# Kernel tuning notes

Hardware: AMD Instinct MI355X
Metric: run time of the kernel (lower is better)

The kernel has to match this reference:

```python
import jax, jax.numpy as jnp
import numpy as np

R0 = 1.0
N_NODES = 10000
N_EDGES = 160000
DIM_A, DIM_V, DIM_D, CHAN = 64, 32, 16, 16

# Levi-Civita tensor for the antisymmetric (cross-product-like) products
_EPS = np.zeros((3, 3, 3), dtype=np.float32)
for (i, j, k), s in (((0,1,2),1.),((1,2,0),1.),((2,0,1),1.),((0,2,1),-1.),((2,1,0),-1.),((1,0,2),-1.)):
    _EPS[i, j, k] = s


def _tl(W, x):
    """TensLinear: mix channel axis 1 of x (B, din, *(3,)*rank) with W (dout, din)."""
    y = jnp.tensordot(x, W, axes=((1,), (1,)))  # (B, *(3,)*rank, dout)
    return jnp.moveaxis(y, -1, 1)


def radial_encode_8(r, r0):
    # 8 Gaussian radial basis functions on |r|/r0
    d = jnp.linalg.norm(r, axis=-1)            # (E,)
    x = d * (8.0 / r0)
    mu = jnp.arange(8, dtype=r.dtype)
    return jnp.exp(-0.5 * (x[:, None] - mu[None, :]) ** 2)  # (E, 8)


def tens_sigmoid_1(v):
    # equivariant squashing: scale vector by tanh(|v|)/|v|
    n = jnp.linalg.norm(v, axis=-1, keepdims=True)
    return v * jnp.tanh(n) / (n + 1e-12)


def _forward(floats, src, dst, n_nodes):
    (r_ij, x_a, x_v, x_d, W_L0, W_L1, W_L2,
     W_Y000, W_Y110, W_Y220, W_Y011, W_Y101, W_Y121, W_Y211,
     W_Y022, W_Y202, W_Y112, W_Y222, W_Y111, W_Y212,
     W_enc, b_enc, W_dir, W1, b1, W2, b2, W3, b3) = floats
    eps = jnp.asarray(_EPS)
    rad = radial_encode_8(r_ij, R0) @ W_enc.T + b_enc        # (E, chan)
    r = tens_sigmoid_1(r_ij * (7.0 / R0))                    # (E, 3)
    phi_a = rad                                              # (E, chan)
    phi_v = rad[:, :, None] * r[:, None, :]                  # (E, chan, 3)
    phi_d = rad[:, :, None, None] * r[:, None, None, :] * r[:, None, :, None]  # (E, chan, 3, 3)
    # gather destination-node features per edge
    x_a_j = _tl(W_L0, x_a)[dst]                              # (E, chan)
    x_v_j = _tl(W_L1, x_v)[dst]                              # (E, chan, 3)
    x_d_j = _tl(W_L2, x_d)[dst]                              # (E, chan, 3, 3)
    # equivariant tensor products (Bee.apply)
    y_000 = x_a_j * phi_a
    y_110 = jnp.sum(x_v_j * phi_v, -1)
    y_220 = jnp.sum(x_d_j * phi_d, (-2, -1))
    y_011 = x_a_j[..., None] * phi_v
    y_101 = x_v_j * phi_a[..., None]
    y_121 = jnp.einsum('ecj,ecji->eci', x_v_j, phi_d)
    y_211 = jnp.einsum('ecij,ecj->eci', x_d_j, phi_v)
    y_022 = x_a_j[..., None, None] * phi_d
    y_202 = x_d_j * phi_a[..., None, None]
    y_112 = x_v_j[..., :, None] * phi_v[..., None, :]
    y_222 = jnp.einsum('ecik,eckj->ecij', x_d_j, phi_d)
    y_111 = jnp.cross(x_v_j, phi_v)
    y_212 = jnp.einsum('ikl,eckj,ecl->ecij', eps, x_d_j, phi_v)
    psi_a = _tl(W_Y000, y_000) + _tl(W_Y110, y_110) + _tl(W_Y220, y_220)
    psi_v = (_tl(W_Y011, y_011) + _tl(W_Y101, y_101) + _tl(W_Y121, y_121)
             + _tl(W_Y211, y_211) + _tl(W_Y111, y_111))
    psi_d = (_tl(W_Y022, y_022) + _tl(W_Y202, y_202) + _tl(W_Y112, y_112)
             + _tl(W_Y222, y_222) + _tl(W_Y212, y_212))
    # residual MLP on the scalar channel: lin_direct(x) + layers(x)
    lrelu = lambda x: jnp.where(x >= 0, x, 0.1 * x)
    h = lrelu(psi_a @ W1.T + b1)
    h = lrelu(h @ W2.T + b2)
    psi_a = psi_a + psi_a @ W_dir.T + (h @ W3.T + b3)
    # scatter-reduce messages to source nodes
    B_a = jax.ops.segment_sum(psi_a, src, num_segments=n_nodes)
    B_v = jax.ops.segment_sum(psi_v, src, num_segments=n_nodes)
    B_d = jax.ops.segment_sum(psi_d, src, num_segments=n_nodes)
    return 0.1 * B_a, 0.1 * B_v, 0.1 * B_d


def setup_inputs() -> dict:
    key = jax.random.key(0)
    ks = jax.random.split(key, 32)
    f32 = jnp.float32
    nrm = lambda k, shape, scale=1.0: scale * jax.random.normal(k, shape, dtype=f32)
    E, N = N_EDGES, N_NODES
    sC = CHAN ** -0.5
    inp = {
        'r_ij': nrm(ks[0], (E, 3)),
        'x_a': nrm(ks[1], (N, DIM_A)),
        'x_v': nrm(ks[2], (N, DIM_V, 3)),
        'x_d': nrm(ks[3], (N, DIM_D, 3, 3)),
        'W_L0': nrm(ks[4], (CHAN, DIM_A), DIM_A ** -0.5),
        'W_L1': nrm(ks[5], (CHAN, DIM_V), DIM_V ** -0.5),
        'W_L2': nrm(ks[6], (CHAN, DIM_D), DIM_D ** -0.5),
        'W_Y000': nrm(ks[7], (DIM_A, CHAN), sC),
        'W_Y110': nrm(ks[8], (DIM_A, CHAN), sC),
        'W_Y220': nrm(ks[9], (DIM_A, CHAN), sC),
        'W_Y011': nrm(ks[10], (DIM_V, CHAN), sC),
        'W_Y101': nrm(ks[11], (DIM_V, CHAN), sC),
        'W_Y121': nrm(ks[12], (DIM_V, CHAN), sC),
        'W_Y211': nrm(ks[13], (DIM_V, CHAN), sC),
        'W_Y022': nrm(ks[14], (DIM_D, CHAN), sC),
        'W_Y202': nrm(ks[15], (DIM_D, CHAN), sC),
        'W_Y112': nrm(ks[16], (DIM_D, CHAN), sC),
        'W_Y222': nrm(ks[17], (DIM_D, CHAN), sC),
        'W_Y111': nrm(ks[18], (DIM_V, CHAN), sC),
        'W_Y212': nrm(ks[19], (DIM_D, CHAN), sC),
        'W_enc': nrm(ks[20], (CHAN, 8), 8 ** -0.5),
        'b_enc': jnp.zeros((CHAN,), f32),
        'W_dir': nrm(ks[21], (DIM_A, DIM_A), DIM_A ** -0.5),
        'W1': nrm(ks[22], (2 * DIM_A, DIM_A), DIM_A ** -0.5),
        'b1': jnp.zeros((2 * DIM_A,), f32),
        'W2': nrm(ks[23], (2 * DIM_A, 2 * DIM_A), (2 * DIM_A) ** -0.5),
        'b2': jnp.zeros((2 * DIM_A,), f32),
        'W3': nrm(ks[24], (DIM_A, 2 * DIM_A), (2 * DIM_A) ** -0.5),
        'b3': jnp.zeros((DIM_A,), f32),
        'src': jax.random.randint(ks[25], (E,), 0, N, dtype=jnp.int32),
        'dst': jax.random.randint(ks[26], (E,), 0, N, dtype=jnp.int32),
        'n_nodes': N,
    }
    return inp


def reference(r_ij, x_a, x_v, x_d, W_L0, W_L1, W_L2, W_Y000, W_Y110, W_Y220,
              W_Y011, W_Y101, W_Y121, W_Y211, W_Y022, W_Y202, W_Y112, W_Y222,
              W_Y111, W_Y212, W_enc, b_enc, W_dir, W1, b1, W2, b2, W3, b3,
              src, dst, n_nodes):
    floats = (r_ij, x_a, x_v, x_d, W_L0, W_L1, W_L2, W_Y000, W_Y110, W_Y220,
              W_Y011, W_Y101, W_Y121, W_Y211, W_Y022, W_Y202, W_Y112, W_Y222,
              W_Y111, W_Y212, W_enc, b_enc, W_dir, W1, b1, W2, b2, W3, b3)
    return _forward(floats, src, dst, n_nodes)
```

## Files before the change

kernel.cpp:

```cpp
#include <hip/hip_runtime.h>
#include <hip/hip_bf16.h>

typedef __hip_bfloat16 bf16;
typedef __attribute__((ext_vector_type(8))) short bf16x8;
typedef __attribute__((ext_vector_type(4))) float f32x4;

__device__ __forceinline__ void st_bf16(short* p, float v) {
    uint32_t u = __float_as_uint(v) + 0x8000u;
    *p = (short)(u >> 16);
}
__device__ __forceinline__ float bb2f(short s) {
    uint32_t u = ((uint32_t)(uint16_t)s) << 16;
    return __uint_as_float(u);
}

__global__ __launch_bounds__(256) void prep_all(
    const float* __restrict__ W000, const float* __restrict__ W110, const float* __restrict__ W220,
    const float* __restrict__ W011, const float* __restrict__ W101, const float* __restrict__ W121,
    const float* __restrict__ W211, const float* __restrict__ W111,
    const float* __restrict__ W022, const float* __restrict__ W202, const float* __restrict__ W112,
    const float* __restrict__ W222, const float* __restrict__ W212,
    const float* __restrict__ W1, const float* __restrict__ W2, const float* __restrict__ W3,
    const float* __restrict__ Wdir, bf16* __restrict__ wout,
    const float* __restrict__ xa, const float* __restrict__ xv, const float* __restrict__ xd,
    const float* __restrict__ WL0, const float* __restrict__ WL1, const float* __restrict__ WL2,
    float* __restrict__ Pa, float* __restrict__ Pv, float* __restrict__ Pd, int N, int NPB,
    const int* __restrict__ src, const int* __restrict__ dst,
    int* __restrict__ cnt_s, int* __restrict__ cnt_d, int E)
{
    int b = blockIdx.x;
    const int tid = threadIdx.x;
    if (b < 178) {
        int i = b * 256 + tid;
        if (i >= 45568) return;
        float v = 0.f;
        if (i < 4096) {
            int o = i >> 6, k = i & 63;
            if (k < 48) {
                int t = k >> 4, c = k & 15;
                const float* W = (t == 0) ? W000 : (t == 1) ? W110 : W220;
                v = W[o * 16 + c];
            }
        } else if (i < 7168) {
            int r = i - 4096, ch = r / 96, k = r % 96;
            if (k < 80) {
                int t = k >> 4, c = k & 15;
                const float* W = (t == 0) ? W011 : (t == 1) ? W101 : (t == 2) ? W121 : (t == 3) ? W211 : W111;
                v = W[ch * 16 + c];
            }
        } else if (i < 8704) {
            int r = i - 7168, ch = r / 96, k = r % 96;
            if (k < 80) {
                int t = k >> 4, c = k & 15;
                const float* W = (t == 0) ? W022 : (t == 1) ? W202 : (t == 2) ? W112 : (t == 3) ? W222 : W212;
                v = W[ch * 16 + c];
            }
        } else if (i < 16896) v = W1[i - 8704];
        else if (i < 33280) v = W2[i - 16896];
        else if (i < 41472) v = W3[i - 33280];
        else v = Wdir[i - 41472];
        wout[i] = __float2bfloat16(v);
        return;
    }
    b -= 178;
    if (b < NPB) {
        __shared__ float sxa[256], sxv[384], sxd[576];
        const int n0 = b * 4;
        if (n0 + tid / 64 < N) sxa[tid] = xa[(size_t)n0 * 64 + tid];
        for (int i = tid; i < 384; i += 256) if (n0 + i / 96 < N)  sxv[i] = xv[(size_t)n0 * 96 + i];
        for (int i = tid; i < 576; i += 256) if (n0 + i / 144 < N) sxd[i] = xd[(size_t)n0 * 144 + i];
        __syncthreads();
        for (int o = tid; o < 832; o += 256) {
            int ln = o / 208, s = o % 208;
            int n = n0 + ln;
            if (n >= N) continue;
            if (s < 16) {
                float a = 0.f;
                const float* w = WL0 + s * 64;
                const float* x = sxa + ln * 64;
                for (int d = 0; d < 64; ++d) a += w[d] * x[d];
                Pa[(size_t)n * 16 + s] = a;
            } else if (s < 64) {
                int idx = s - 16, c = idx / 3, i = idx % 3;
                float a = 0.f;
                const float* w = WL1 + c * 32;
                const float* x = sxv + ln * 96;
                for (int d = 0; d < 32; ++d) a += w[d] * x[d * 3 + i];
                Pv[(size_t)n * 64 + c * 4 + i] = a;
            } else {
                int idx = s - 64, c = idx / 9, ij = idx % 9;
                float a = 0.f;
                const float* w = WL2 + c * 16;
                const float* x = sxd + ln * 144;
                for (int d = 0; d < 16; ++d) a += w[d] * x[d * 9 + ij];
                Pd[(size_t)n * 192 + c * 12 + ij] = a;
            }
        }
        return;
    }
    b -= NPB;
    int i = b * 256 + tid;
    if (i < E) {
        atomicAdd(&cnt_s[src[i]], 1);
        atomicAdd(&cnt_d[dst[i]], 1);
    }
}

__global__ void scan_rows2(const int* __restrict__ cnt_s, int* __restrict__ rs_s,
                           const int* __restrict__ cnt_d, int* __restrict__ rs_d, int N) {
    const int* cnt = blockIdx.x ? cnt_d : cnt_s;
    int* rowstart = blockIdx.x ? rs_d : rs_s;
    __shared__ int ps[256];
    int t = threadIdx.x;
    int chunk = (N + 255) / 256;
    int base = t * chunk;
    int s = 0;
    for (int i = 0; i < chunk; ++i) { int idx = base + i; if (idx < N) s += cnt[idx]; }
    ps[t] = s;
    __syncthreads();
    for (int off = 1; off < 256; off <<= 1) {
        int v = (t >= off) ? ps[t - off] : 0;
        __syncthreads();
        ps[t] += v;
        __syncthreads();
    }
    int run = (t > 0) ? ps[t - 1] : 0;
    for (int i = 0; i < chunk; ++i) {
        int idx = base + i;
        if (idx < N) { rowstart[idx] = run; run += cnt[idx]; }
    }
    if (t == 255) rowstart[N] = run;
}

__global__ void fill_slot(const int* __restrict__ src, const int* __restrict__ dst,
                          const int* __restrict__ rs_s, const int* __restrict__ rs_d,
                          int* __restrict__ cur_s, int* __restrict__ cur_d,
                          int* __restrict__ slot, int* __restrict__ eperm, int E) {
    int i = blockIdx.x * 256 + threadIdx.x;
    if (i < E) {
        slot[i] = rs_s[src[i]] + atomicAdd(&cur_s[src[i]], 1);
        int p = rs_d[dst[i]] + atomicAdd(&cur_d[dst[i]], 1);
        eperm[p] = i;
    }
}

__global__ __launch_bounds__(256) void edge_mfma(
    const float* __restrict__ r_ij,
    const float* __restrict__ Pa, const float* __restrict__ Pv, const float* __restrict__ Pd,
    const float* __restrict__ Wenc, const float* __restrict__ benc,
    const bf16* __restrict__ Wa, const bf16* __restrict__ Wv, const bf16* __restrict__ Wd,
    const bf16* __restrict__ Wb1, const bf16* __restrict__ Wb2,
    const bf16* __restrict__ Wb3, const bf16* __restrict__ Wbdir,
    const float* __restrict__ b1, const float* __restrict__ b2, const float* __restrict__ b3,
    const int* __restrict__ slot, const int* __restrict__ dst,
    const int* __restrict__ eperm,
    short* __restrict__ psi, int E, int nwg)
{
    __shared__ __align__(16) char smem[32320];
    short* SYA   = (short*)smem;
    short* SYV   = (short*)(smem + 1536);
    short* SYD   = (short*)(smem + 9216);
    int*   SSLOT = (int*)(smem + 32256);
    short* SPSIA = (short*)(smem + 1536);
    short* SH1   = (short*)(smem + 3840);
    short* SH2   = (short*)(smem + 8192);
    short* SPSI  = (short*)(smem + 12544);

    const int tid = threadIdx.x;
    int orig = blockIdx.x;
    int q = nwg >> 3, r = nwg & 7;
    int xcd = orig & 7, idx = orig >> 3;
    int tile = (xcd < r) ? (xcd * (q + 1) + idx) : (r * (q + 1) + (xcd - r) * q + idx);
    const int e0 = tile * 16;
    const bf16x8 z8 = {};

    {
        const int le = tid >> 4, c = tid & 15;
        if (e0 + le < E) {
            const int e = eperm[e0 + le];
            const int j = dst[e];
            if (c == 0) SSLOT[le] = slot[e];
            float vx = 7.f * r_ij[e * 3 + 0];
            float vy = 7.f * r_ij[e * 3 + 1];
            float vz = 7.f * r_ij[e * 3 + 2];
            float nn = sqrtf(vx * vx + vy * vy + vz * vz);
            float ex = __expf(-2.f * nn);
            float th = (1.f - ex) * __builtin_amdgcn_rcpf(1.f + ex);
            float sc = th * __builtin_amdgcn_rcpf(nn + 1e-12f);
            float rr[3] = {vx * sc, vy * sc, vz * sc};
            float x8 = nn * (8.f / 7.f);
            float rad = benc[c];
            #pragma unroll
            for (int m = 0; m < 8; ++m) {
                float tt = x8 - (float)m;
                rad += __expf(-0.5f * tt * tt) * Wenc[c * 8 + m];
            }
            float xa = Pa[j * 16 + c];
            f32x4 pv4 = *(const f32x4*)(Pv + (size_t)j * 64 + c * 4);
            f32x4 pd0 = *(const f32x4*)(Pd + (size_t)j * 192 + c * 12);
            f32x4 pd1 = *(const f32x4*)(Pd + (size_t)j * 192 + c * 12 + 4);
            f32x4 pd2 = *(const f32x4*)(Pd + (size_t)j * 192 + c * 12 + 8);
            float xv[3] = {pv4[0], pv4[1], pv4[2]};
            float xd[9] = {pd0[0], pd0[1], pd0[2], pd0[3], pd1[0], pd1[1], pd1[2], pd1[3], pd2[0]};
            float dotv = xv[0] * rr[0] + xv[1] * rr[1] + xv[2] * rr[2];
            float mv[3];
            #pragma unroll
            for (int i = 0; i < 3; ++i)
                mv[i] = xd[i * 3] * rr[0] + xd[i * 3 + 1] * rr[1] + xd[i * 3 + 2] * rr[2];
            float quad = mv[0] * rr[0] + mv[1] * rr[1] + mv[2] * rr[2];
            st_bf16(&SYA[le * 48 + c],      xa * rad);
            st_bf16(&SYA[le * 48 + 16 + c], rad * dotv);
            st_bf16(&SYA[le * 48 + 32 + c], rad * quad);
            #pragma unroll
            for (int i = 0; i < 3; ++i) {
                int row = (le * 3 + i) * 80;
                int i1 = (i + 1) % 3, i2 = (i + 2) % 3;
                st_bf16(&SYV[row + c],      xa * rad * rr[i]);
                st_bf16(&SYV[row + 16 + c], rad * xv[i]);
                st_bf16(&SYV[row + 32 + c], rad * dotv * rr[i]);
                st_bf16(&SYV[row + 48 + c], rad * mv[i]);
                st_bf16(&SYV[row + 64 + c], rad * (xv[i1] * rr[i2] - xv[i2] * rr[i1]));
            }
            #pragma unroll
            for (int i = 0; i < 3; ++i) {
                int i1 = (i + 1) % 3, i2 = (i + 2) % 3;
                #pragma unroll
                for (int jj = 0; jj < 3; ++jj) {
                    int row = (le * 9 + i * 3 + jj) * 80;
                    st_bf16(&SYD[row + c],      xa * rad * rr[i] * rr[jj]);
                    st_bf16(&SYD[row + 16 + c], rad * xd[i * 3 + jj]);
                    st_bf16(&SYD[row + 32 + c], rad * xv[i] * rr[jj]);
                    st_bf16(&SYD[row + 48 + c], rad * mv[i] * rr[jj]);
                    st_bf16(&SYD[row + 64 + c], rad * (xd[i1 * 3 + jj] * rr[i2] - xd[i2 * 3 + jj] * rr[i1]));
                }
            }
        }
    }
    __syncthreads();

    const int wid = tid >> 6, lane = tid & 63;
    const int q16 = lane >> 4, r16 = lane & 15;

    f32x4 da[4] = {};
    f32x4 dv[3][2] = {};
    f32x4 dd[5] = {};
    const int mstart = (wid == 2) ? 0 : 5;
    const int mcnt = (wid == 2) ? 5 : 4;

    if (wid == 0) {
        bf16x8 af0 = *(const bf16x8*)&SYA[r16 * 48 + q16 * 8];
        bf16x8 af1 = z8;
        if (q16 < 2) af1 = *(const bf16x8*)&SYA[r16 * 48 + 32 + q16 * 8];
        #pragma unroll
        for (int n = 0; n < 4; ++n) {
            bf16x8 bf0 = *(const bf16x8*)((const short*)Wa + (n * 16 + r16) * 64 + q16 * 8);
            bf16x8 bf1 = *(const bf16x8*)((const short*)Wa + (n * 16 + r16) * 64 + 32 + q16 * 8);
            da[n] = __builtin_amdgcn_mfma_f32_16x16x32_bf16(af0, bf0, da[n], 0, 0, 0);
            da[n] = __builtin_amdgcn_mfma_f32_16x16x32_bf16(af1, bf1, da[n], 0, 0, 0);
        }
    } else if (wid == 1) {
        #pragma unroll
        for (int ks = 0; ks < 3; ++ks) {
            bf16x8 av[3], bv[2];
            #pragma unroll
            for (int m = 0; m < 3; ++m) {
                if (ks < 2) av[m] = *(const bf16x8*)&SYV[(m * 16 + r16) * 80 + ks * 32 + q16 * 8];
                else {
                    av[m] = z8;
                    if (q16 < 2) av[m] = *(const bf16x8*)&SYV[(m * 16 + r16) * 80 + 64 + q16 * 8];
                }
            }
            #pragma unroll
            for (int n = 0; n < 2; ++n)
                bv[n] = *(const bf16x8*)((const short*)Wv + (n * 16 + r16) * 96 + ks * 32 + q16 * 8);
            #pragma unroll
            for (int m = 0; m < 3; ++m)
                #pragma unroll
                for (int n = 0; n < 2; ++n)
                    dv[m][n] = __builtin_amdgcn_mfma_f32_16x16x32_bf16(av[m], bv[n], dv[m][n], 0, 0, 0);
        }
    } else {
        #pragma unroll
        for (int ks = 0; ks < 3; ++ks) {
            bf16x8 bf = *(const bf16x8*)((const short*)Wd + r16 * 96 + ks * 32 + q16 * 8);
            for (int mi = 0; mi < mcnt; ++mi) {
                bf16x8 af;
                if (ks < 2) af = *(const bf16x8*)&SYD[((mstart + mi) * 16 + r16) * 80 + ks * 32 + q16 * 8];
                else {
                    af = z8;
                    if (q16 < 2) af = *(const bf16x8*)&SYD[((mstart + mi) * 16 + r16) * 80 + 64 + q16 * 8];
                }
                dd[mi] = __builtin_amdgcn_mfma_f32_16x16x32_bf16(af, bf, dd[mi], 0, 0, 0);
            }
        }
    }
    __syncthreads();

    if (wid == 0) {
        #pragma unroll
        for (int n = 0; n < 4; ++n)
            #pragma unroll
            for (int jj = 0; jj < 4; ++jj)
                st_bf16(&SPSIA[(q16 * 4 + jj) * 72 + n * 16 + r16], da[n][jj]);
    } else if (wid == 1) {
        #pragma unroll
        for (int m = 0; m < 3; ++m)
            #pragma unroll
            for (int n = 0; n < 2; ++n)
                #pragma unroll
                for (int jj = 0; jj < 4; ++jj) {
                    int row = m * 16 + q16 * 4 + jj;
                    int el = row / 3, i = row % 3;
                    st_bf16(&SPSI[el * 304 + 64 + (n * 16 + r16) * 3 + i], dv[m][n][jj]);
                }
    } else {
        for (int mi = 0; mi < mcnt; ++mi)
            #pragma unroll
            for (int jj = 0; jj < 4; ++jj) {
                int row = (mstart + mi) * 16 + q16 * 4 + jj;
                int el = row / 9, ij = row % 9;
                st_bf16(&SPSI[el * 304 + 160 + r16 * 9 + ij], dd[mi][jj]);
            }
    }
    __syncthreads();

    {
        f32x4 h1a[2] = {};
        #pragma unroll
        for (int ks = 0; ks < 2; ++ks) {
            bf16x8 af = *(const bf16x8*)&SPSIA[r16 * 72 + ks * 32 + q16 * 8];
            #pragma unroll
            for (int n = 0; n < 2; ++n) {
                int col = wid * 32 + n * 16 + r16;
                bf16x8 bf = *(const bf16x8*)((const short*)Wb1 + col * 64 + ks * 32 + q16 * 8);
                h1a[n] = __builtin_amdgcn_mfma_f32_16x16x32_bf16(af, bf, h1a[n], 0, 0, 0);
            }
        }
        #pragma unroll
        for (int n = 0; n < 2; ++n) {
            int col = wid * 32 + n * 16 + r16;
            float bias = b1[col];
            #pragma unroll
            for (int jj = 0; jj < 4; ++jj) {
                float v = h1a[n][jj] + bias;
                v = v >= 0.f ? v : 0.1f * v;
                st_bf16(&SH1[(q16 * 4 + jj) * 136 + col], v);
            }
        }
    }
    __syncthreads();
    {
        f32x4 h2a[2] = {};
        #pragma unroll
        for (int ks = 0; ks < 4; ++ks) {
            bf16x8 af = *(const bf16x8*)&SH1[r16 * 136 + ks * 32 + q16 * 8];
            #pragma unroll
            for (int n = 0; n < 2; ++n) {
                int col = wid * 32 + n * 16 + r16;
                bf16x8 bf = *(const bf16x8*)((const short*)Wb2 + col * 128 + ks * 32 + q16 * 8);
                h2a[n] = __builtin_amdgcn_mfma_f32_16x16x32_bf16(af, bf, h2a[n], 0, 0, 0);
            }
        }
        #pragma unroll
        for (int n = 0; n < 2; ++n) {
            int col = wid * 32 + n * 16 + r16;
            float bias = b2[col];
            #pragma unroll
            for (int jj = 0; jj < 4; ++jj) {
                float v = h2a[n][jj] + bias;
                v = v >= 0.f ? v : 0.1f * v;
                st_bf16(&SH2[(q16 * 4 + jj) * 136 + col], v);
            }
        }
    }
    __syncthreads();
    {
        f32x4 o3 = {};
        const int col3 = wid * 16 + r16;
        #pragma unroll
        for (int ks = 0; ks < 4; ++ks) {
            bf16x8 af = *(const bf16x8*)&SH2[r16 * 136 + ks * 32 + q16 * 8];
            bf16x8 bf = *(const bf16x8*)((const short*)Wb3 + col3 * 128 + ks * 32 + q16 * 8);
            o3 = __builtin_amdgcn_mfma_f32_16x16x32_bf16(af, bf, o3, 0, 0, 0);
        }
        #pragma unroll
        for (int ks = 0; ks < 2; ++ks) {
            bf16x8 af = *(const bf16x8*)&SPSIA[r16 * 72 + ks * 32 + q16 * 8];
            bf16x8 bf = *(const bf16x8*)((const short*)Wbdir + col3 * 64 + ks * 32 + q16 * 8);
            o3 = __builtin_amdgcn_mfma_f32_16x16x32_bf16(af, bf, o3, 0, 0, 0);
        }
        float bias = b3[col3];
        #pragma unroll
        for (int jj = 0; jj < 4; ++jj) {
            int row = q16 * 4 + jj;
            float v = o3[jj] + bias + bb2f(SPSIA[row * 72 + col3]);
            st_bf16(&SPSI[row * 304 + col3], v);
        }
    }
    __syncthreads();

    {
        const uint32_t* S32 = (const uint32_t*)SPSI;
        uint32_t* P32 = (uint32_t*)psi;
        for (int idx2 = tid; idx2 < 16 * 152; idx2 += 256) {
            int le = idx2 / 152, k = idx2 - le * 152;
            if (e0 + le < E)
                P32[(size_t)SSLOT[le] * 152 + k] = S32[le * 152 + k];
        }
    }
}

__global__ __launch_bounds__(128) void gather(
    const short* __restrict__ psi, const int* __restrict__ rowstart,
    float* __restrict__ out, int N) {
    int n = blockIdx.x, t = threadIdx.x;
    if (t >= 76) return;
    int s0 = rowstart[n], s1 = rowstart[n + 1];
    float a0 = 0.f, a1 = 0.f, a2 = 0.f, a3 = 0.f;
    for (int s = s0; s < s1; ++s) {
        const uint32_t* p = (const uint32_t*)(psi + (size_t)s * 304) + 2 * t;
        uint32_t u0 = p[0], u1 = p[1];
        a0 += __uint_as_float(u0 << 16);
        a1 += __uint_as_float(u0 & 0xffff0000u);
        a2 += __uint_as_float(u1 << 16);
        a3 += __uint_as_float(u1 & 0xffff0000u);
    }
    int f = 4 * t;
    f32x4 v = {0.1f * a0, 0.1f * a1, 0.1f * a2, 0.1f * a3};
    if (f < 64)       *(f32x4*)&out[(size_t)n * 64 + f] = v;
    else if (f < 160) *(f32x4*)&out[(size_t)N * 64 + (size_t)n * 96 + (f - 64)] = v;
    else              *(f32x4*)&out[(size_t)N * 160 + (size_t)n * 144 + (f - 160)] = v;
}

extern "C" void kernel_launch(void* const* d_in, const int* in_sizes, int n_in,
                              void* d_out, int out_size, void* d_ws, size_t ws_size,
                              hipStream_t stream) {
    const float* r_ij = (const float*)d_in[0];
    const float* x_a  = (const float*)d_in[1];
    const float* x_v  = (const float*)d_in[2];
    const float* x_d  = (const float*)d_in[3];
    const float* W_L0 = (const float*)d_in[4];
    const float* W_L1 = (const float*)d_in[5];
    const float* W_L2 = (const float*)d_in[6];
    const float* W000 = (const float*)d_in[7];
    const float* W110 = (const float*)d_in[8];
    const float* W220 = (const float*)d_in[9];
    const float* W011 = (const float*)d_in[10];
    const float* W101 = (const float*)d_in[11];
    const float* W121 = (const float*)d_in[12];
    const float* W211 = (const float*)d_in[13];
    const float* W022 = (const float*)d_in[14];
    const float* W202 = (const float*)d_in[15];
    const float* W112 = (const float*)d_in[16];
    const float* W222 = (const float*)d_in[17];
    const float* W111 = (const float*)d_in[18];
    const float* W212 = (const float*)d_in[19];
    const float* Wenc = (const float*)d_in[20];
    const float* benc = (const float*)d_in[21];
    const float* Wdir = (const float*)d_in[22];
    const float* W1   = (const float*)d_in[23];
    const float* b1   = (const float*)d_in[24];
    const float* W2   = (const float*)d_in[25];
    const float* b2   = (const float*)d_in[26];
    const float* W3   = (const float*)d_in[27];
    const float* b3   = (const float*)d_in[28];
    const int* src    = (const int*)d_in[29];
    const int* dst    = (const int*)d_in[30];

    const int E = in_sizes[29];
    const int N = in_sizes[1] / 64;

    float* Pa     = (float*)d_ws;
    float* Pv     = Pa + (size_t)N * 16;
    float* Pd     = Pv + (size_t)N * 64;
    bf16*  Wb     = (bf16*)(Pd + (size_t)N * 192);
    int*   cnt_s  = (int*)(Wb + 45568);
    int*   cur_s  = cnt_s + N;
    int*   cnt_d  = cur_s + N;
    int*   cur_d  = cnt_d + N;
    int*   rs_s   = cur_d + N;
    int*   rs_d   = rs_s + N + 1;
    int*   slot   = rs_d + N + 1;
    int*   eperm  = slot + E;
    short* psi    = (short*)(eperm + E);

    const bf16* Wa_p    = Wb;
    const bf16* Wv_p    = Wb + 4096;
    const bf16* Wd_p    = Wb + 7168;
    const bf16* Wb1_p   = Wb + 8704;
    const bf16* Wb2_p   = Wb + 16896;
    const bf16* Wb3_p   = Wb + 33280;
    const bf16* Wbdir_p = Wb + 41472;

    const int NPB = (N + 3) / 4;
    const int HB  = (E + 255) / 256;
    const int nwg = (E + 15) / 16;

    hipMemsetAsync(cnt_s, 0, (size_t)4 * N * sizeof(int), stream);
    prep_all<<<178 + NPB + HB, 256, 0, stream>>>(
        W000, W110, W220, W011, W101, W121, W211, W111,
        W022, W202, W112, W222, W212, W1, W2, W3, Wdir, Wb,
        x_a, x_v, x_d, W_L0, W_L1, W_L2, Pa, Pv, Pd, N, NPB,
        src, dst, cnt_s, cnt_d, E);
    scan_rows2<<<2, 256, 0, stream>>>(cnt_s, rs_s, cnt_d, rs_d, N);
    fill_slot<<<HB, 256, 0, stream>>>(src, dst, rs_s, rs_d, cur_s, cur_d, slot, eperm, E);
    edge_mfma<<<nwg, 256, 0, stream>>>(
        r_ij, Pa, Pv, Pd, Wenc, benc,
        Wa_p, Wv_p, Wd_p, Wb1_p, Wb2_p, Wb3_p, Wbdir_p,
        b1, b2, b3, slot, dst, eperm, psi, E, nwg);
    gather<<<N, 128, 0, stream>>>(psi, rs_s, (float*)d_out, N);
}
```

Baseline: 253.9 us.

## Make each wave process its own four edges independently, removing block barriers

Each 16-edge tile is split so that every wavefront owns 4 edges and its own LDS region. The tensor-product and MLP stages run entirely within one wave, so all `__syncthreads` between stages go away. The cost is that each wave now issues full 16-row MFMAs for the whole MLP while only 4 rows hold real data, which multiplies matrix work per edge. A launch-bounds occupancy hint of 5 is also added.

Result: slower. 512.8 us (+102.0%).

```diff
diff --git a/kernel.cpp b/kernel.cpp
--- a/kernel.cpp
+++ b/kernel.cpp
@@ -144,7 +144,7 @@
     }
 }
 
-__global__ __launch_bounds__(256) void edge_mfma(
+__global__ __launch_bounds__(256, 5) void edge_mfma(
     const float* __restrict__ r_ij,
     const float* __restrict__ Pa, const float* __restrict__ Pv, const float* __restrict__ Pd,
     const float* __restrict__ Wenc, const float* __restrict__ benc,
@@ -157,27 +157,29 @@
     short* __restrict__ psi, int E, int nwg)
 {
     __shared__ __align__(16) char smem[32320];
-    short* SYA   = (short*)smem;
-    short* SYV   = (short*)(smem + 1536);
-    short* SYD   = (short*)(smem + 9216);
-    int*   SSLOT = (int*)(smem + 32256);
-    short* SPSIA = (short*)(smem + 1536);
-    short* SH1   = (short*)(smem + 3840);
-    short* SH2   = (short*)(smem + 8192);
-    short* SPSI  = (short*)(smem + 12544);
-
     const int tid = threadIdx.x;
+    const int wid = tid >> 6, lane = tid & 63;
+    short* wb = (short*)(smem + wid * 8080);
+    short* SYA   = wb;
+    short* SYV   = wb + 192;
+    short* SYD   = wb + 1152;
+    int*   SSLOT = (int*)((char*)wb + 8064);
+    short* SPSIA = wb + 192;
+    short* SH1   = wb + 480;
+    short* SH2   = wb + 1024;
+    short* SPSI  = wb + 2816;
+
     int orig = blockIdx.x;
-    int q = nwg >> 3, r = nwg & 7;
-    int xcd = orig & 7, idx = orig >> 3;
-    int tile = (xcd < r) ? (xcd * (q + 1) + idx) : (r * (q + 1) + (xcd - r) * q + idx);
-    const int e0 = tile * 16;
+    int qn = nwg >> 3, rn = nwg & 7;
+    int xcd = orig & 7, tidx = orig >> 3;
+    int tile = (xcd < rn) ? (xcd * (qn + 1) + tidx) : (rn * (qn + 1) + (xcd - rn) * qn + tidx);
+    const int ebase = tile * 16 + wid * 4;
     const bf16x8 z8 = {};
 
     {
-        const int le = tid >> 4, c = tid & 15;
-        if (e0 + le < E) {
-            const int e = eperm[e0 + le];
+        const int le = lane >> 4, c = lane & 15;
+        if (ebase + le < E) {
+            const int e = eperm[ebase + le];
             const int j = dst[e];
             if (c == 0) SSLOT[le] = slot[e];
             float vx = 7.f * r_ij[e * 3 + 0];
@@ -236,18 +238,13 @@
             }
         }
     }
-    __syncthreads();
-
-    const int wid = tid >> 6, lane = tid & 63;
+
     const int q16 = lane >> 4, r16 = lane & 15;
 
     f32x4 da[4] = {};
-    f32x4 dv[3][2] = {};
-    f32x4 dd[5] = {};
-    const int mstart = (wid == 2) ? 0 : 5;
-    const int mcnt = (wid == 2) ? 5 : 4;
-
-    if (wid == 0) {
+    f32x4 dv[2] = {};
+    f32x4 dd[3] = {};
+    {
         bf16x8 af0 = *(const bf16x8*)&SYA[r16 * 48 + q16 * 8];
         bf16x8 af1 = z8;
         if (q16 < 2) af1 = *(const bf16x8*)&SYA[r16 * 48 + 32 + q16 * 8];
@@ -258,153 +255,167 @@
             da[n] = __builtin_amdgcn_mfma_f32_16x16x32_bf16(af0, bf0, da[n], 0, 0, 0);
             da[n] = __builtin_amdgcn_mfma_f32_16x16x32_bf16(af1, bf1, da[n], 0, 0, 0);
         }
-    } else if (wid == 1) {
+    }
+    {
         #pragma unroll
         for (int ks = 0; ks < 3; ++ks) {
-            bf16x8 av[3], bv[2];
-            #pragma unroll
-            for (int m = 0; m < 3; ++m) {
-                if (ks < 2) av[m] = *(const bf16x8*)&SYV[(m * 16 + r16) * 80 + ks * 32 + q16 * 8];
-                else {
-                    av[m] = z8;
-                    if (q16 < 2) av[m] = *(const bf16x8*)&SYV[(m * 16 + r16) * 80 + 64 + q16 * 8];
-                }
-            }
-            #pragma unroll
-            for (int n = 0; n < 2; ++n)
-                bv[n] = *(const bf16x8*)((const short*)Wv + (n * 16 + r16) * 96 + ks * 32 + q16 * 8);
-            #pragma unroll
-            for (int m = 0; m < 3; ++m)
-                #pragma unroll
-                for (int n = 0; n < 2; ++n)
-                    dv[m][n] = __builtin_amdgcn_mfma_f32_16x16x32_bf16(av[m], bv[n], dv[m][n], 0, 0, 0);
-        }
-    } else {
+            bf16x8 av;
+            if (ks < 2) av = *(const bf16x8*)&SYV[r16 * 80 + ks * 32 + q16 * 8];
+            else {
+                av = z8;
+                if (q16 < 2) av = *(const bf16x8*)&SYV[r16 * 80 + 64 + q16 * 8];
+            }
+            #pragma unroll
+            for (int n = 0; n < 2; ++n) {
+                bf16x8 bv = *(const bf16x8*)((const short*)Wv + (n * 16 + r16) * 96 + ks * 32 + q16 * 8);
+                dv[n] = __builtin_amdgcn_mfma_f32_16x16x32_bf16(av, bv, dv[n], 0, 0, 0);
+            }
+        }
+    }
+    {
+        const int mrow[3] = {0, 16, 20};
         #pragma unroll
         for (int ks = 0; ks < 3; ++ks) {
             bf16x8 bf = *(const bf16x8*)((const short*)Wd + r16 * 96 + ks * 32 + q16 * 8);
-            for (int mi = 0; mi < mcnt; ++mi) {
+            #pragma unroll
+            for (int mi = 0; mi < 3; ++mi) {
                 bf16x8 af;
-                if (ks < 2) af = *(const bf16x8*)&SYD[((mstart + mi) * 16 + r16) * 80 + ks * 32 + q16 * 8];
+                if (ks < 2) af = *(const bf16x8*)&SYD[(mrow[mi] + r16) * 80 + ks * 32 + q16 * 8];
                 else {
                     af = z8;
-                    if (q16 < 2) af = *(const bf16x8*)&SYD[((mstart + mi) * 16 + r16) * 80 + 64 + q16 * 8];
+                    if (q16 < 2) af = *(const bf16x8*)&SYD[(mrow[mi] + r16) * 80 + 64 + q16 * 8];
                 }
                 dd[mi] = __builtin_amdgcn_mfma_f32_16x16x32_bf16(af, bf, dd[mi], 0, 0, 0);
             }
         }
     }
-    __syncthreads();
-
-    if (wid == 0) {
+
+    if (q16 == 0) {
         #pragma unroll
         for (int n = 0; n < 4; ++n)
             #pragma unroll
             for (int jj = 0; jj < 4; ++jj)
-                st_bf16(&SPSIA[(q16 * 4 + jj) * 72 + n * 16 + r16], da[n][jj]);
-    } else if (wid == 1) {
-        #pragma unroll
-        for (int m = 0; m < 3; ++m)
-            #pragma unroll
-            for (int n = 0; n < 2; ++n)
+                st_bf16(&SPSIA[jj * 72 + n * 16 + r16], da[n][jj]);
+    }
+    if (q16 < 3) {
+        #pragma unroll
+        for (int n = 0; n < 2; ++n)
+            #pragma unroll
+            for (int jj = 0; jj < 4; ++jj) {
+                int row = q16 * 4 + jj;
+                int el = row / 3, i = row % 3;
+                st_bf16(&SPSI[el * 304 + 64 + (n * 16 + r16) * 3 + i], dv[n][jj]);
+            }
+    }
+    {
+        const int mrow[3] = {0, 16, 20};
+        #pragma unroll
+        for (int mi = 0; mi < 3; ++mi) {
+            if (mi == 2 && q16 != 3) continue;
+            #pragma unroll
+            for (int jj = 0; jj < 4; ++jj) {
+                int grow = mrow[mi] + q16 * 4 + jj;
+                if (mi == 2) grow = 32 + jj;
+                int el = grow / 9, ij = grow % 9;
+                st_bf16(&SPSI[el * 304 + 160 + r16 * 9 + ij], dd[mi][jj]);
+            }
+        }
+    }
+
+    {
+        f32x4 h1a[8] = {};
+        #pragma unroll
+        for (int ks = 0; ks < 2; ++ks) {
+            bf16x8 af = *(const bf16x8*)&SPSIA[r16 * 72 + ks * 32 + q16 * 8];
+            #pragma unroll
+            for (int n = 0; n < 8; ++n) {
+                int col = n * 16 + r16;
+                bf16x8 bf = *(const bf16x8*)((const short*)Wb1 + col * 64 + ks * 32 + q16 * 8);
+                h1a[n] = __builtin_amdgcn_mfma_f32_16x16x32_bf16(af, bf, h1a[n], 0, 0, 0);
+            }
+        }
+        if (q16 == 0) {
+            #pragma unroll
+            for (int n = 0; n < 8; ++n) {
+                int col = n * 16 + r16;
+                float bias = b1[col];
                 #pragma unroll
                 for (int jj = 0; jj < 4; ++jj) {
-                    int row = m * 16 + q16 * 4 + jj;
-                    int el = row / 3, i = row % 3;
-                    st_bf16(&SPSI[el * 304 + 64 + (n * 16 + r16) * 3 + i], dv[m][n][jj]);
+                    float v = h1a[n][jj] + bias;
+                    v = v >= 0.f ? v : 0.1f * v;
+                    st_bf16(&SH1[jj * 136 + col], v);
                 }
-    } else {
-        for (int mi = 0; mi < mcnt; ++mi)
-            #pragma unroll
-            for (int jj = 0; jj < 4; ++jj) {
-                int row = (mstart + mi) * 16 + q16 * 4 + jj;
-                int el = row / 9, ij = row % 9;
-                st_bf16(&SPSI[el * 304 + 160 + r16 * 9 + ij], dd[mi][jj]);
-            }
-    }
-    __syncthreads();
-
-    {
-        f32x4 h1a[2] = {};
+            }
+        }
+    }
+    {
+        f32x4 h2a[8] = {};
+        #pragma unroll
+        for (int ks = 0; ks < 4; ++ks) {
+            bf16x8 af = *(const bf16x8*)&SH1[r16 * 136 + ks * 32 + q16 * 8];
+            #pragma unroll
+            for (int n = 0; n < 8; ++n) {
+                int col = n * 16 + r16;
+                bf16x8 bf = *(const bf16x8*)((const short*)Wb2 + col * 128 + ks * 32 + q16 * 8);
+                h2a[n] = __builtin_amdgcn_mfma_f32_16x16x32_bf16(af, bf, h2a[n], 0, 0, 0);
+            }
+        }
+        if (q16 == 0) {
+            #pragma unroll
+            for (int n = 0; n < 8; ++n) {
+                int col = n * 16 + r16;
+                float bias = b2[col];
+                #pragma unroll
+                for (int jj = 0; jj < 4; ++jj) {
+                    float v = h2a[n][jj] + bias;
+                    v = v >= 0.f ? v : 0.1f * v;
+                    st_bf16(&SH2[jj * 136 + col], v);
+                }
+            }
+        }
+    }
+    {
+        f32x4 o3[4] = {};
+        #pragma unroll
+        for (int ks = 0; ks < 4; ++ks) {
+            bf16x8 af = *(const bf16x8*)&SH2[r16 * 136 + ks * 32 + q16 * 8];
+            #pragma unroll
+            for (int n = 0; n < 4; ++n) {
+                int col = n * 16 + r16;
+                bf16x8 bf = *(const bf16x8*)((const short*)Wb3 + col * 128 + ks * 32 + q16 * 8);
+                o3[n] = __builtin_amdgcn_mfma_f32_16x16x32_bf16(af, bf, o3[n], 0, 0, 0);
+            }
+        }
         #pragma unroll
         for (int ks = 0; ks < 2; ++ks) {
             bf16x8 af = *(const bf16x8*)&SPSIA[r16 * 72 + ks * 32 + q16 * 8];
             #pragma unroll
-            for (int n = 0; n < 2; ++n) {
-                int col = wid * 32 + n * 16 + r16;
-                bf16x8 bf = *(const bf16x8*)((const short*)Wb1 + col * 64 + ks * 32 + q16 * 8);
-                h1a[n] = __builtin_amdgcn_mfma_f32_16x16x32_bf16(af, bf, h1a[n], 0, 0, 0);
-            }
-        }
-        #pragma unroll
-        for (int n = 0; n < 2; ++n) {
-            int col = wid * 32 + n * 16 + r16;
-            float bias = b1[col];
-            #pragma unroll
-            for (int jj = 0; jj < 4; ++jj) {
-                float v = h1a[n][jj] + bias;
-                v = v >= 0.f ? v : 0.1f * v;
-                st_bf16(&SH1[(q16 * 4 + jj) * 136 + col], v);
-            }
-        }
-    }
-    __syncthreads();
-    {
-        f32x4 h2a[2] = {};
-        #pragma unroll
-        for (int ks = 0; ks < 4; ++ks) {
-            bf16x8 af = *(const bf16x8*)&SH1[r16 * 136 + ks * 32 + q16 * 8];
-            #pragma unroll
-            for (int n = 0; n < 2; ++n) {
-                int col = wid * 32 + n * 16 + r16;
-                bf16x8 bf = *(const bf16x8*)((const short*)Wb2 + col * 128 + ks * 32 + q16 * 8);
-                h2a[n] = __builtin_amdgcn_mfma_f32_16x16x32_bf16(af, bf, h2a[n], 0, 0, 0);
-            }
-        }
-        #pragma unroll
-        for (int n = 0; n < 2; ++n) {
-            int col = wid * 32 + n * 16 + r16;
-            float bias = b2[col];
-            #pragma unroll
-            for (int jj = 0; jj < 4; ++jj) {
-                float v = h2a[n][jj] + bias;
-                v = v >= 0.f ? v : 0.1f * v;
-                st_bf16(&SH2[(q16 * 4 + jj) * 136 + col], v);
-            }
-        }
-    }
-    __syncthreads();
-    {
-        f32x4 o3 = {};
-        const int col3 = wid * 16 + r16;
-        #pragma unroll
-        for (int ks = 0; ks < 4; ++ks) {
-            bf16x8 af = *(const bf16x8*)&SH2[r16 * 136 + ks * 32 + q16 * 8];
-            bf16x8 bf = *(const bf16x8*)((const short*)Wb3 + col3 * 128 + ks * 32 + q16 * 8);
-            o3 = __builtin_amdgcn_mfma_f32_16x16x32_bf16(af, bf, o3, 0, 0, 0);
-        }
-        #pragma unroll
-        for (int ks = 0; ks < 2; ++ks) {
-            bf16x8 af = *(const bf16x8*)&SPSIA[r16 * 72 + ks * 32 + q16 * 8];
-            bf16x8 bf = *(const bf16x8*)((const short*)Wbdir + col3 * 64 + ks * 32 + q16 * 8);
-            o3 = __builtin_amdgcn_mfma_f32_16x16x32_bf16(af, bf, o3, 0, 0, 0);
-        }
-        float bias = b3[col3];
-        #pragma unroll
-        for (int jj = 0; jj < 4; ++jj) {
-            int row = q16 * 4 + jj;
-            float v = o3[jj] + bias + bb2f(SPSIA[row * 72 + col3]);
-            st_bf16(&SPSI[row * 304 + col3], v);
-        }
-    }
-    __syncthreads();
+            for (int n = 0; n < 4; ++n) {
+                int col = n * 16 + r16;
+                bf16x8 bf = *(const bf16x8*)((const short*)Wbdir + col * 64 + ks * 32 + q16 * 8);
+                o3[n] = __builtin_amdgcn_mfma_f32_16x16x32_bf16(af, bf, o3[n], 0, 0, 0);
+            }
+        }
+        if (q16 == 0) {
+            #pragma unroll
+            for (int n = 0; n < 4; ++n) {
+                int col = n * 16 + r16;
+                float bias = b3[col];
+                #pragma unroll
+                for (int jj = 0; jj < 4; ++jj) {
+                    float v = o3[n][jj] + bias + bb2f(SPSIA[jj * 72 + col]);
+                    st_bf16(&SPSI[jj * 304 + col], v);
+                }
+            }
+        }
+    }
 
     {
         const uint32_t* S32 = (const uint32_t*)SPSI;
         uint32_t* P32 = (uint32_t*)psi;
-        for (int idx2 = tid; idx2 < 16 * 152; idx2 += 256) {
-            int le = idx2 / 152, k = idx2 - le * 152;
-            if (e0 + le < E)
+        for (int idx = lane; idx < 608; idx += 64) {
+            int le = idx / 152, k = idx - le * 152;
+            if (ebase + le < E)
                 P32[(size_t)SSLOT[le] * 152 + k] = S32[le * 152 + k];
         }
     }
```

## Make edge kernel persistent with software-prefetched gathers across tiles

Applied to the files above, without the earlier changes.

Switches edge_mfma from one 16-edge tile per block to a fixed grid of 1280 blocks that each loop over a contiguous chunk of tiles. The gathered per-edge inputs (eperm, dst, slot, r_ij, projected node features) for the next tile are loaded into registers while the current tile is computed, to hide global-load latency and amortise block launch overhead. It adds a trailing barrier per tile, increases register pressure, sets a min-blocks-per-CU launch bound, and drops the previous XCD-aware tile remapping, which may change L2 locality.

Result: slower. 436.0 us (+71.7%).

```diff
diff --git a/kernel.cpp b/kernel.cpp
--- a/kernel.cpp
+++ b/kernel.cpp
@@ -144,7 +144,7 @@
     }
 }
 
-__global__ __launch_bounds__(256) void edge_mfma(
+__global__ __launch_bounds__(256, 5) void edge_mfma(
     const float* __restrict__ r_ij,
     const float* __restrict__ Pa, const float* __restrict__ Pv, const float* __restrict__ Pd,
     const float* __restrict__ Wenc, const float* __restrict__ benc,
@@ -154,7 +154,7 @@
     const float* __restrict__ b1, const float* __restrict__ b2, const float* __restrict__ b3,
     const int* __restrict__ slot, const int* __restrict__ dst,
     const int* __restrict__ eperm,
-    short* __restrict__ psi, int E, int nwg)
+    short* __restrict__ psi, int E, int TT, int chunk)
 {
     __shared__ __align__(16) char smem[32320];
     short* SYA   = (short*)smem;
@@ -167,22 +167,52 @@
     short* SPSI  = (short*)(smem + 12544);
 
     const int tid = threadIdx.x;
-    int orig = blockIdx.x;
-    int q = nwg >> 3, r = nwg & 7;
-    int xcd = orig & 7, idx = orig >> 3;
-    int tile = (xcd < r) ? (xcd * (q + 1) + idx) : (r * (q + 1) + (xcd - r) * q + idx);
-    const int e0 = tile * 16;
+    const int wid = tid >> 6, lane = tid & 63;
+    const int q16 = lane >> 4, r16 = lane & 15;
+    const int le = tid >> 4, c = tid & 15;
     const bf16x8 z8 = {};
 
-    {
-        const int le = tid >> 4, c = tid & 15;
-        if (e0 + le < E) {
-            const int e = eperm[e0 + le];
-            const int j = dst[e];
-            if (c == 0) SSLOT[le] = slot[e];
-            float vx = 7.f * r_ij[e * 3 + 0];
-            float vy = 7.f * r_ij[e * 3 + 1];
-            float vz = 7.f * r_ij[e * 3 + 2];
+    const int tstart = blockIdx.x * chunk;
+    const int tend = min(TT, tstart + chunk);
+    if (tstart >= tend) return;
+
+    bool nvalid = false;
+    int nsl = 0;
+    float nr0 = 0.f, nr1 = 0.f, nr2 = 0.f, npa = 0.f;
+    f32x4 npv = {}, npd0 = {}, npd1 = {}, npd2 = {};
+
+    #define DO_PREFETCH(TILE)                                              \
+        {                                                                   \
+            int eb = (TILE) * 16 + le;                                      \
+            nvalid = (eb < E);                                              \
+            if (nvalid) {                                                   \
+                int e_ = eperm[eb];                                         \
+                int j_ = dst[e_];                                           \
+                nsl = slot[e_];                                             \
+                nr0 = r_ij[e_ * 3 + 0];                                     \
+                nr1 = r_ij[e_ * 3 + 1];                                     \
+                nr2 = r_ij[e_ * 3 + 2];                                     \
+                npa = Pa[j_ * 16 + c];                                      \
+                npv = *(const f32x4*)(Pv + (size_t)j_ * 64 + c * 4);        \
+                npd0 = *(const f32x4*)(Pd + (size_t)j_ * 192 + c * 12);     \
+                npd1 = *(const f32x4*)(Pd + (size_t)j_ * 192 + c * 12 + 4); \
+                npd2 = *(const f32x4*)(Pd + (size_t)j_ * 192 + c * 12 + 8); \
+            }                                                               \
+        }
+
+    DO_PREFETCH(tstart);
+
+    for (int t = tstart; t < tend; ++t) {
+        const int e0 = t * 16;
+        const bool valid = nvalid;
+        const int sl = nsl;
+        const float cr0 = nr0, cr1 = nr1, cr2 = nr2, cpa = npa;
+        const f32x4 cpv = npv, cpd0 = npd0, cpd1 = npd1, cpd2 = npd2;
+        if (t + 1 < tend) DO_PREFETCH(t + 1);
+
+        if (valid) {
+            if (c == 0) SSLOT[le] = sl;
+            float vx = 7.f * cr0, vy = 7.f * cr1, vz = 7.f * cr2;
             float nn = sqrtf(vx * vx + vy * vy + vz * vz);
             float ex = __expf(-2.f * nn);
             float th = (1.f - ex) * __builtin_amdgcn_rcpf(1.f + ex);
@@ -195,13 +225,10 @@
                 float tt = x8 - (float)m;
                 rad += __expf(-0.5f * tt * tt) * Wenc[c * 8 + m];
             }
-            float xa = Pa[j * 16 + c];
-            f32x4 pv4 = *(const f32x4*)(Pv + (size_t)j * 64 + c * 4);
-            f32x4 pd0 = *(const f32x4*)(Pd + (size_t)j * 192 + c * 12);
-            f32x4 pd1 = *(const f32x4*)(Pd + (size_t)j * 192 + c * 12 + 4);
-            f32x4 pd2 = *(const f32x4*)(Pd + (size_t)j * 192 + c * 12 + 8);
-            float xv[3] = {pv4[0], pv4[1], pv4[2]};
-            float xd[9] = {pd0[0], pd0[1], pd0[2], pd0[3], pd1[0], pd1[1], pd1[2], pd1[3], pd2[0]};
+            float xa = cpa;
+            float xv[3] = {cpv[0], cpv[1], cpv[2]};
+            float xd[9] = {cpd0[0], cpd0[1], cpd0[2], cpd0[3],
+                           cpd1[0], cpd1[1], cpd1[2], cpd1[3], cpd2[0]};
             float dotv = xv[0] * rr[0] + xv[1] * rr[1] + xv[2] * rr[2];
             float mv[3];
             #pragma unroll
@@ -235,179 +262,178 @@
                 }
             }
         }
-    }
-    __syncthreads();
-
-    const int wid = tid >> 6, lane = tid & 63;
-    const int q16 = lane >> 4, r16 = lane & 15;
-
-    f32x4 da[4] = {};
-    f32x4 dv[3][2] = {};
-    f32x4 dd[5] = {};
-    const int mstart = (wid == 2) ? 0 : 5;
-    const int mcnt = (wid == 2) ? 5 : 4;
-
-    if (wid == 0) {
-        bf16x8 af0 = *(const bf16x8*)&SYA[r16 * 48 + q16 * 8];
-        bf16x8 af1 = z8;
-        if (q16 < 2) af1 = *(const bf16x8*)&SYA[r16 * 48 + 32 + q16 * 8];
-        #pragma unroll
-        for (int n = 0; n < 4; ++n) {
-            bf16x8 bf0 = *(const bf16x8*)((const short*)Wa + (n * 16 + r16) * 64 + q16 * 8);
-            bf16x8 bf1 = *(const bf16x8*)((const short*)Wa + (n * 16 + r16) * 64 + 32 + q16 * 8);
-            da[n] = __builtin_amdgcn_mfma_f32_16x16x32_bf16(af0, bf0, da[n], 0, 0, 0);
-            da[n] = __builtin_amdgcn_mfma_f32_16x16x32_bf16(af1, bf1, da[n], 0, 0, 0);
-        }
-    } else if (wid == 1) {
-        #pragma unroll
-        for (int ks = 0; ks < 3; ++ks) {
-            bf16x8 av[3], bv[2];
-            #pragma unroll
-            for (int m = 0; m < 3; ++m) {
-                if (ks < 2) av[m] = *(const bf16x8*)&SYV[(m * 16 + r16) * 80 + ks * 32 + q16 * 8];
-                else {
-                    av[m] = z8;
-                    if (q16 < 2) av[m] = *(const bf16x8*)&SYV[(m * 16 + r16) * 80 + 64 + q16 * 8];
-                }
-            }
-            #pragma unroll
-            for (int n = 0; n < 2; ++n)
-                bv[n] = *(const bf16x8*)((const short*)Wv + (n * 16 + r16) * 96 + ks * 32 + q16 * 8);
+        __syncthreads();
+
+        f32x4 da[4] = {};
+        f32x4 dv[3][2] = {};
+        f32x4 dd[5] = {};
+        const int mstart = (wid == 2) ? 0 : 5;
+        const int mcnt = (wid == 2) ? 5 : 4;
+
+        if (wid == 0) {
+            bf16x8 af0 = *(const bf16x8*)&SYA[r16 * 48 + q16 * 8];
+            bf16x8 af1 = z8;
+            if (q16 < 2) af1 = *(const bf16x8*)&SYA[r16 * 48 + 32 + q16 * 8];
+            #pragma unroll
+            for (int n = 0; n < 4; ++n) {
+                bf16x8 bf0 = *(const bf16x8*)((const short*)Wa + (n * 16 + r16) * 64 + q16 * 8);
+                bf16x8 bf1 = *(const bf16x8*)((const short*)Wa + (n * 16 + r16) * 64 + 32 + q16 * 8);
+                da[n] = __builtin_amdgcn_mfma_f32_16x16x32_bf16(af0, bf0, da[n], 0, 0, 0);
+                da[n] = __builtin_amdgcn_mfma_f32_16x16x32_bf16(af1, bf1, da[n], 0, 0, 0);
+            }
+        } else if (wid == 1) {
+            #pragma unroll
+            for (int ks = 0; ks < 3; ++ks) {
+                bf16x8 av[3], bv[2];
+                #pragma unroll
+                for (int m = 0; m < 3; ++m) {
+                    if (ks < 2) av[m] = *(const bf16x8*)&SYV[(m * 16 + r16) * 80 + ks * 32 + q16 * 8];
+                    else {
+                        av[m] = z8;
+                        if (q16 < 2) av[m] = *(const bf16x8*)&SYV[(m * 16 + r16) * 80 + 64 + q16 * 8];
+                    }
+                }
+                #pragma unroll
+                for (int n = 0; n < 2; ++n)
+                    bv[n] = *(const bf16x8*)((const short*)Wv + (n * 16 + r16) * 96 + ks * 32 + q16 * 8);
+                #pragma unroll
+                for (int m = 0; m < 3; ++m)
+                    #pragma unroll
+                    for (int n = 0; n < 2; ++n)
+                        dv[m][n] = __builtin_amdgcn_mfma_f32_16x16x32_bf16(av[m], bv[n], dv[m][n], 0, 0, 0);
+            }
+        } else {
+            #pragma unroll
+            for (int ks = 0; ks < 3; ++ks) {
+                bf16x8 bf = *(const bf16x8*)((const short*)Wd + r16 * 96 + ks * 32 + q16 * 8);
+                for (int mi = 0; mi < mcnt; ++mi) {
+                    bf16x8 af;
+                    if (ks < 2) af = *(const bf16x8*)&SYD[((mstart + mi) * 16 + r16) * 80 + ks * 32 + q16 * 8];
+                    else {
+                        af = z8;
+                        if (q16 < 2) af = *(const bf16x8*)&SYD[((mstart + mi) * 16 + r16) * 80 + 64 + q16 * 8];
+                    }
+                    dd[mi] = __builtin_amdgcn_mfma_f32_16x16x32_bf16(af, bf, dd[mi], 0, 0, 0);
+                }
+            }
+        }
+        __syncthreads();
+
+        if (wid == 0) {
+            #pragma unroll
+            for (int n = 0; n < 4; ++n)
+                #pragma unroll
+                for (int jj = 0; jj < 4; ++jj)
+                    st_bf16(&SPSIA[(q16 * 4 + jj) * 72 + n * 16 + r16], da[n][jj]);
+        } else if (wid == 1) {
             #pragma unroll
             for (int m = 0; m < 3; ++m)
                 #pragma unroll
                 for (int n = 0; n < 2; ++n)
-                    dv[m][n] = __builtin_amdgcn_mfma_f32_16x16x32_bf16(av[m], bv[n], dv[m][n], 0, 0, 0);
-        }
-    } else {
-        #pragma unroll
-        for (int ks = 0; ks < 3; ++ks) {
-            bf16x8 bf = *(const bf16x8*)((const short*)Wd + r16 * 96 + ks * 32 + q16 * 8);
-            for (int mi = 0; mi < mcnt; ++mi) {
-                bf16x8 af;
-                if (ks < 2) af = *(const bf16x8*)&SYD[((mstart + mi) * 16 + r16) * 80 + ks * 32 + q16 * 8];
-                else {
-                    af = z8;
-                    if (q16 < 2) af = *(const bf16x8*)&SYD[((mstart + mi) * 16 + r16) * 80 + 64 + q16 * 8];
-                }
-                dd[mi] = __builtin_amdgcn_mfma_f32_16x16x32_bf16(af, bf, dd[mi], 0, 0, 0);
-            }
-        }
-    }
-    __syncthreads();
-
-    if (wid == 0) {
-        #pragma unroll
-        for (int n = 0; n < 4; ++n)
-            #pragma unroll
-            for (int jj = 0; jj < 4; ++jj)
-                st_bf16(&SPSIA[(q16 * 4 + jj) * 72 + n * 16 + r16], da[n][jj]);
-    } else if (wid == 1) {
-        #pragma unroll
-        for (int m = 0; m < 3; ++m)
-            #pragma unroll
-            for (int n = 0; n < 2; ++n)
+                    #pragma unroll
+                    for (int jj = 0; jj < 4; ++jj) {
+                        int row = m * 16 + q16 * 4 + jj;
+                        int el = row / 3, i = row % 3;
+                        st_bf16(&SPSI[el * 304 + 64 + (n * 16 + r16) * 3 + i], dv[m][n][jj]);
+                    }
+        } else {
+            for (int mi = 0; mi < mcnt; ++mi)
                 #pragma unroll
                 for (int jj = 0; jj < 4; ++jj) {
-                    int row = m * 16 + q16 * 4 + jj;
-                    int el = row / 3, i = row % 3;
-                    st_bf16(&SPSI[el * 304 + 64 + (n * 16 + r16) * 3 + i], dv[m][n][jj]);
-                }
-    } else {
-        for (int mi = 0; mi < mcnt; ++mi)
-            #pragma unroll
-            for (int jj = 0; jj < 4; ++jj) {
-                int row = (mstart + mi) * 16 + q16 * 4 + jj;
-                int el = row / 9, ij = row % 9;
-                st_bf16(&SPSI[el * 304 + 160 + r16 * 9 + ij], dd[mi][jj]);
-            }
-    }
-    __syncthreads();
-
-    {
-        f32x4 h1a[2] = {};
-        #pragma unroll
-        for (int ks = 0; ks < 2; ++ks) {
-            bf16x8 af = *(const bf16x8*)&SPSIA[r16 * 72 + ks * 32 + q16 * 8];
+                    int row = (mstart + mi) * 16 + q16 * 4 + jj;
+                    int el = row / 9, ij = row % 9;
+                    st_bf16(&SPSI[el * 304 + 160 + r16 * 9 + ij], dd[mi][jj]);
+                }
+        }
+        __syncthreads();
+
+        {
+            f32x4 h1a[2] = {};
+            #pragma unroll
+            for (int ks = 0; ks < 2; ++ks) {
+                bf16x8 af = *(const bf16x8*)&SPSIA[r16 * 72 + ks * 32 + q16 * 8];
+                #pragma unroll
+                for (int n = 0; n < 2; ++n) {
+                    int col = wid * 32 + n * 16 + r16;
+                    bf16x8 bf = *(const bf16x8*)((const short*)Wb1 + col * 64 + ks * 32 + q16 * 8);
+                    h1a[n] = __builtin_amdgcn_mfma_f32_16x16x32_bf16(af, bf, h1a[n], 0, 0, 0);
+                }
+            }
             #pragma unroll
             for (int n = 0; n < 2; ++n) {
                 int col = wid * 32 + n * 16 + r16;
-                bf16x8 bf = *(const bf16x8*)((const short*)Wb1 + col * 64 + ks * 32 + q16 * 8);
-                h1a[n] = __builtin_amdgcn_mfma_f32_16x16x32_bf16(af, bf, h1a[n], 0, 0, 0);
-            }
-        }
-        #pragma unroll
-        for (int n = 0; n < 2; ++n) {
-            int col = wid * 32 + n * 16 + r16;
-            float bias = b1[col];
-            #pragma unroll
-            for (int jj = 0; jj < 4; ++jj) {
-                float v = h1a[n][jj] + bias;
-                v = v >= 0.f ? v : 0.1f * v;
-                st_bf16(&SH1[(q16 * 4 + jj) * 136 + col], v);
-            }
-        }
-    }
-    __syncthreads();
-    {
-        f32x4 h2a[2] = {};
-        #pragma unroll
-        for (int ks = 0; ks < 4; ++ks) {
-            bf16x8 af = *(const bf16x8*)&SH1[r16 * 136 + ks * 32 + q16 * 8];
+                float bias = b1[col];
+                #pragma unroll
+                for (int jj = 0; jj < 4; ++jj) {
+                    float v = h1a[n][jj] + bias;
+                    v = v >= 0.f ? v : 0.1f * v;
+                    st_bf16(&SH1[(q16 * 4 + jj) * 136 + col], v);
+                }
+            }
+        }
+        __syncthreads();
+        {
+            f32x4 h2a[2] = {};
+            #pragma unroll
+            for (int ks = 0; ks < 4; ++ks) {
+                bf16x8 af = *(const bf16x8*)&SH1[r16 * 136 + ks * 32 + q16 * 8];
+                #pragma unroll
+                for (int n = 0; n < 2; ++n) {
+                    int col = wid * 32 + n * 16 + r16;
+                    bf16x8 bf = *(const bf16x8*)((const short*)Wb2 + col * 128 + ks * 32 + q16 * 8);
+                    h2a[n] = __builtin_amdgcn_mfma_f32_16x16x32_bf16(af, bf, h2a[n], 0, 0, 0);
+                }
+            }
             #pragma unroll
             for (int n = 0; n < 2; ++n) {
                 int col = wid * 32 + n * 16 + r16;
-                bf16x8 bf = *(const bf16x8*)((const short*)Wb2 + col * 128 + ks * 32 + q16 * 8);
-                h2a[n] = __builtin_amdgcn_mfma_f32_16x16x32_bf16(af, bf, h2a[n], 0, 0, 0);
-            }
-        }
-        #pragma unroll
-        for (int n = 0; n < 2; ++n) {
-            int col = wid * 32 + n * 16 + r16;
-            float bias = b2[col];
+                float bias = b2[col];
+                #pragma unroll
+                for (int jj = 0; jj < 4; ++jj) {
+                    float v = h2a[n][jj] + bias;
+                    v = v >= 0.f ? v : 0.1f * v;
+                    st_bf16(&SH2[(q16 * 4 + jj) * 136 + col], v);
+                }
+            }
+        }
+        __syncthreads();
+        {
+            f32x4 o3 = {};
+            const int col3 = wid * 16 + r16;
+            #pragma unroll
+            for (int ks = 0; ks < 4; ++ks) {
+                bf16x8 af = *(const bf16x8*)&SH2[r16 * 136 + ks * 32 + q16 * 8];
+                bf16x8 bf = *(const bf16x8*)((const short*)Wb3 + col3 * 128 + ks * 32 + q16 * 8);
+                o3 = __builtin_amdgcn_mfma_f32_16x16x32_bf16(af, bf, o3, 0, 0, 0);
+            }
+            #pragma unroll
+            for (int ks = 0; ks < 2; ++ks) {
+                bf16x8 af = *(const bf16x8*)&SPSIA[r16 * 72 + ks * 32 + q16 * 8];
+                bf16x8 bf = *(const bf16x8*)((const short*)Wbdir + col3 * 64 + ks * 32 + q16 * 8);
+                o3 = __builtin_amdgcn_mfma_f32_16x16x32_bf16(af, bf, o3, 0, 0, 0);
+            }
+            float bias = b3[col3];
             #pragma unroll
             for (int jj = 0; jj < 4; ++jj) {
-                float v = h2a[n][jj] + bias;
-                v = v >= 0.f ? v : 0.1f * v;
-                st_bf16(&SH2[(q16 * 4 + jj) * 136 + col], v);
-            }
-        }
-    }
-    __syncthreads();
-    {
-        f32x4 o3 = {};
-        const int col3 = wid * 16 + r16;
-        #pragma unroll
-        for (int ks = 0; ks < 4; ++ks) {
-            bf16x8 af = *(const bf16x8*)&SH2[r16 * 136 + ks * 32 + q16 * 8];
-            bf16x8 bf = *(const bf16x8*)((const short*)Wb3 + col3 * 128 + ks * 32 + q16 * 8);
-            o3 = __builtin_amdgcn_mfma_f32_16x16x32_bf16(af, bf, o3, 0, 0, 0);
-        }
-        #pragma unroll
-        for (int ks = 0; ks < 2; ++ks) {
-            bf16x8 af = *(const bf16x8*)&SPSIA[r16 * 72 + ks * 32 + q16 * 8];
-            bf16x8 bf = *(const bf16x8*)((const short*)Wbdir + col3 * 64 + ks * 32 + q16 * 8);
-            o3 = __builtin_amdgcn_mfma_f32_16x16x32_bf16(af, bf, o3, 0, 0, 0);
-        }
-        float bias = b3[col3];
-        #pragma unroll
-        for (int jj = 0; jj < 4; ++jj) {
-            int row = q16 * 4 + jj;
-            float v = o3[jj] + bias + bb2f(SPSIA[row * 72 + col3]);
-            st_bf16(&SPSI[row * 304 + col3], v);
-        }
-    }
-    __syncthreads();
-
-    {
-        const uint32_t* S32 = (const uint32_t*)SPSI;
-        uint32_t* P32 = (uint32_t*)psi;
-        for (int idx2 = tid; idx2 < 16 * 152; idx2 += 256) {
-            int le = idx2 / 152, k = idx2 - le * 152;
-            if (e0 + le < E)
-                P32[(size_t)SSLOT[le] * 152 + k] = S32[le * 152 + k];
-        }
-    }
+                int row = q16 * 4 + jj;
+                float v = o3[jj] + bias + bb2f(SPSIA[row * 72 + col3]);
+                st_bf16(&SPSI[row * 304 + col3], v);
+            }
+        }
+        __syncthreads();
+
+        {
+            const uint32_t* S32 = (const uint32_t*)SPSI;
+            uint32_t* P32 = (uint32_t*)psi;
+            for (int idx2 = tid; idx2 < 16 * 152; idx2 += 256) {
+                int lee = idx2 / 152, k = idx2 - lee * 152;
+                if (e0 + lee < E)
+                    P32[(size_t)SSLOT[lee] * 152 + k] = S32[lee * 152 + k];
+            }
+        }
+        __syncthreads();
+    }
+    #undef DO_PREFETCH
 }
 
 __global__ __launch_bounds__(128) void gather(
@@ -494,7 +520,9 @@
 
     const int NPB = (N + 3) / 4;
     const int HB  = (E + 255) / 256;
-    const int nwg = (E + 15) / 16;
+    const int TT  = (E + 15) / 16;
+    const int G   = 1280;
+    const int chunk = (TT + G - 1) / G;
 
     hipMemsetAsync(cnt_s, 0, (size_t)4 * N * sizeof(int), stream);
     prep_all<<<178 + NPB + HB, 256, 0, stream>>>(
@@ -504,9 +532,9 @@
         src, dst, cnt_s, cnt_d, E);
     scan_rows2<<<2, 256, 0, stream>>>(cnt_s, rs_s, cnt_d, rs_d, N);
     fill_slot<<<HB, 256, 0, stream>>>(src, dst, rs_s, rs_d, cur_s, cur_d, slot, eperm, E);
-    edge_mfma<<<nwg, 256, 0, stream>>>(
+    edge_mfma<<<G, 256, 0, stream>>>(
         r_ij, Pa, Pv, Pd, Wenc, benc,
         Wa_p, Wv_p, Wd_p, Wb1_p, Wb2_p, Wb3_p, Wbdir_p,
-        b1, b2, b3, slot, dst, eperm, psi, E, nwg);
+        b1, b2, b3, slot, dst, eperm, psi, E, TT, chunk);
     gather<<<N, 128, 0, stream>>>(psi, rs_s, (float*)d_out, N);
 }
```
